# Optimization experiments

Hardware: AMD Instinct MI355X
Metric: run time of the kernel (lower is better)

Reference implementation:

```python
import jax, jax.numpy as jnp
import numpy as np

N = 50000
IN_CH = 256
HEADS = 8
OUT_CH = 32
E = 800000


def setup_inputs() -> dict:
    key = jax.random.key(0)
    k1, k2, k3, k4, k5 = jax.random.split(key, 5)
    x = jax.random.normal(k1, (N, IN_CH), dtype=jnp.float32)
    edge_index = jax.random.randint(k2, (2, E), 0, N, dtype=jnp.int64)
    # torch Linear(in, heads*out, bias=False): weight [heads*out, in]
    W = jax.random.normal(k3, (HEADS * OUT_CH, IN_CH), dtype=jnp.float32) / np.sqrt(IN_CH)
    # xavier_uniform over (1, heads, out)
    bound = float(np.sqrt(6.0 / (HEADS + OUT_CH)))
    attn_l = jax.random.uniform(k4, (1, HEADS, OUT_CH), minval=-bound, maxval=bound, dtype=jnp.float32)
    attn_r = jax.random.uniform(k5, (1, HEADS, OUT_CH), minval=-bound, maxval=bound, dtype=jnp.float32)
    return {"x": x, "edge_index": edge_index, "W": W, "attn_l": attn_l, "attn_r": attn_r}


def reference(x, edge_index, W, attn_l, attn_r):
    num_nodes = x.shape[0]
    # node-level projection: [N, H, C]
    xp = (x @ W.T).reshape(num_nodes, HEADS, OUT_CH).astype(jnp.float32)
    # add self loops
    loops = jnp.arange(num_nodes, dtype=edge_index.dtype)
    src = jnp.concatenate([edge_index[0], loops])
    dst = jnp.concatenate([edge_index[1], loops])
    # edge attention logits per head: [Etot, H]
    alpha_l = (xp * attn_l).sum(-1)[src]
    alpha_r = (xp * attn_r).sum(-1)[dst]
    alpha = jax.nn.leaky_relu(alpha_l + alpha_r, negative_slope=0.2)
    # global per-head max subtraction (as in the original), then scatter softmax over dst
    alpha = jnp.exp(alpha - alpha.max(axis=0, keepdims=True))
    alpha_sum = jax.ops.segment_sum(alpha, dst, num_segments=num_nodes)  # [N, H]
    alpha = alpha / jnp.maximum(alpha_sum[dst], 1e-6)
    # weighted aggregation: scatter-add alpha * x_src to dst, all heads at once
    msgs = alpha[:, :, None] * xp[src]  # [Etot, H, C]
    out = jax.ops.segment_sum(msgs, dst, num_segments=num_nodes)  # [N, H, C]
    return out.reshape(num_nodes, HEADS * OUT_CH)
```

## Files before the change

kernel.cpp:

```cpp
#include <hip/hip_runtime.h>
#include <math.h>

#define IN_CH   256
#define HEADS   8
#define OUT_CH  32
#define CAP     64

typedef __attribute__((ext_vector_type(8))) short s16x8;
typedef __attribute__((ext_vector_type(4))) float f32x4;

__device__ inline short f2bf(float f) {
  unsigned u = __builtin_bit_cast(unsigned, f);
  u += 0x7fffu + ((u >> 16) & 1u);
  return (short)(u >> 16);
}

__global__ __launch_bounds__(256) void prep(
    const float* __restrict__ W, short* __restrict__ Wb,
    int* __restrict__ cnt) {
  const int b = blockIdx.x;
  if (b < 64) {
    const int i = (b * 256 + (int)threadIdx.x) * 4;
    float4 v = *(const float4*)(W + i);
    ushort4 o;
    o.x = (unsigned short)f2bf(v.x);
    o.y = (unsigned short)f2bf(v.y);
    o.z = (unsigned short)f2bf(v.z);
    o.w = (unsigned short)f2bf(v.w);
    *(ushort4*)(Wb + i) = o;
  } else {
    const int i = ((b - 64) * 256 + (int)threadIdx.x) * 4;
    *(int4*)(cnt + i) = make_int4(0, 0, 0, 0);
  }
}

__global__ __launch_bounds__(256) void gemm_fill(
    const float* __restrict__ x, const short* __restrict__ Wb,
    const float* __restrict__ attn_l, const float* __restrict__ attn_r,
    short* __restrict__ xpb, float* __restrict__ al, float* __restrict__ ar,
    const int* __restrict__ src_idx, const int* __restrict__ dst_idx,
    int* __restrict__ cnt, int* __restrict__ csrs, int E, int n) {
  const int tid = threadIdx.x;

  {
    const int Etot = E + n;
    const int stride = (int)gridDim.x * 256;
    for (int e = (int)blockIdx.x * 256 + tid; e < Etot; e += stride) {
      int s, d;
      if (e < E) {
        s = src_idx[e];
        d = dst_idx[e];
      } else {
        s = d = e - E;
      }
      const int p = atomicAdd(&cnt[d], 1);
      if (p < CAP) csrs[d * CAP + p] = s;
    }
  }

  __shared__ short Ws[8 * 256 * 8];
  __shared__ short Xs[8 * 64 * 8];
  const int wave = tid >> 6;
  const int lane = tid & 63;
  const int nrow = lane & 15;
  const int kq   = lane >> 4;
  const int node0 = blockIdx.x * 64;

  f32x4 acc[4][4];
#pragma unroll
  for (int i = 0; i < 4; ++i)
#pragma unroll
    for (int j = 0; j < 4; ++j) acc[i][j] = (f32x4){0.f, 0.f, 0.f, 0.f};

  for (int k0 = 0; k0 < IN_CH; k0 += 64) {
    __syncthreads();
#pragma unroll
    for (int s = 0; s < 8; ++s) {
      s16x8 v = *(const s16x8*)(Wb + (size_t)tid * IN_CH + k0 + s * 8);
      *(s16x8*)&Ws[(s * 256 + tid) * 8] = v;
    }
#pragma unroll
    for (int p = 0; p < 2; ++p) {
      const int c = p * 256 + tid;
      const int row = c >> 3, o = c & 7;
      int grow = node0 + row;
      if (grow >= n) grow = n - 1;
      const float* xr = x + (size_t)grow * IN_CH + k0 + o * 8;
      float4 lo = *(const float4*)xr;
      float4 hi = *(const float4*)(xr + 4);
      s16x8 v;
      v[0] = f2bf(lo.x); v[1] = f2bf(lo.y); v[2] = f2bf(lo.z); v[3] = f2bf(lo.w);
      v[4] = f2bf(hi.x); v[5] = f2bf(hi.y); v[6] = f2bf(hi.z); v[7] = f2bf(hi.w);
      *(s16x8*)&Xs[(o * 64 + row) * 8] = v;
    }
    __syncthreads();
#pragma unroll
    for (int kk = 0; kk < 2; ++kk) {
      const int o = kk * 4 + kq;
      s16x8 af[4], bf[4];
#pragma unroll
      for (int i = 0; i < 4; ++i)
        af[i] = *(const s16x8*)&Ws[(o * 256 + wave * 64 + i * 16 + nrow) * 8];
#pragma unroll
      for (int j = 0; j < 4; ++j)
        bf[j] = *(const s16x8*)&Xs[(o * 64 + j * 16 + nrow) * 8];
#pragma unroll
      for (int i = 0; i < 4; ++i)
#pragma unroll
        for (int j = 0; j < 4; ++j)
          acc[i][j] = __builtin_amdgcn_mfma_f32_16x16x32_bf16(
              af[i], bf[j], acc[i][j], 0, 0, 0);
    }
  }

  float pl[4][2] = {}, pr[4][2] = {};
#pragma unroll
  for (int i = 0; i < 4; ++i) {
    const int oc = wave * 64 + i * 16 + kq * 4;
    const float4 la = *(const float4*)(attn_l + oc);
    const float4 ra = *(const float4*)(attn_r + oc);
    const int hh = i >> 1;
#pragma unroll
    for (int j = 0; j < 4; ++j) {
      const int node = node0 + j * 16 + nrow;
      ushort4 st;
      st.x = (unsigned short)f2bf(acc[i][j][0]);
      st.y = (unsigned short)f2bf(acc[i][j][1]);
      st.z = (unsigned short)f2bf(acc[i][j][2]);
      st.w = (unsigned short)f2bf(acc[i][j][3]);
      if (node < n) *(ushort4*)(xpb + (size_t)node * IN_CH + oc) = st;
      pl[j][hh] += acc[i][j][0] * la.x + acc[i][j][1] * la.y +
                   acc[i][j][2] * la.z + acc[i][j][3] * la.w;
      pr[j][hh] += acc[i][j][0] * ra.x + acc[i][j][1] * ra.y +
                   acc[i][j][2] * ra.z + acc[i][j][3] * ra.w;
    }
  }
#pragma unroll
  for (int j = 0; j < 4; ++j)
#pragma unroll
    for (int hh = 0; hh < 2; ++hh) {
      float vl = pl[j][hh], vr = pr[j][hh];
      vl += __shfl_xor(vl, 16); vl += __shfl_xor(vl, 32);
      vr += __shfl_xor(vr, 16); vr += __shfl_xor(vr, 32);
      const int node = node0 + j * 16 + nrow;
      if (kq == 0 && node < n) {
        al[node * HEADS + wave * 2 + hh] = vl;
        ar[node * HEADS + wave * 2 + hh] = vr;
      }
    }
}

__device__ inline void acc8(float w, const s16x8& u, float* acc) {
  const unsigned* p = (const unsigned*)&u;
#pragma unroll
  for (int j = 0; j < 4; ++j) {
    const unsigned v = p[j];
    const float flo = __builtin_bit_cast(float, v << 16);
    const float fhi = __builtin_bit_cast(float, v & 0xFFFF0000u);
    acc[2 * j]     = fmaf(w, flo, acc[2 * j]);
    acc[2 * j + 1] = fmaf(w, fhi, acc[2 * j + 1]);
  }
}

__global__ __launch_bounds__(256) void gat_gather(
    const int* __restrict__ csrs, const int* __restrict__ cntp,
    const short* __restrict__ xpb, const float* __restrict__ al,
    const float* __restrict__ ar, float* __restrict__ out, int n) {
  const int gid = blockIdx.x * blockDim.x + threadIdx.x;
  const int d = gid >> 6;
  if (d >= n) return;
  const int lane = gid & 63;
  const int half = lane >> 5;
  const int cl = lane & 31;
  const int h = cl >> 2;
  const int start = d * CAP;
  int cnt = cntp[d];
  if (cnt > CAP) cnt = CAP;
  const float ard = ar[d * HEADS + h];

  float acc[8] = {0.f, 0.f, 0.f, 0.f, 0.f, 0.f, 0.f, 0.f};
  float denom = 0.f;
  for (int jb = 0; jb < cnt; jb += 8) {
    const int base = jb + half * 4;
    const int4 q = *(const int4*)(csrs + start + base);
    const int* qp = (const int*)&q;
    int s[4];
#pragma unroll
    for (int i = 0; i < 4; ++i) s[i] = (base + i < cnt) ? qp[i] : d;
    s16x8 u[4];
#pragma unroll
    for (int i = 0; i < 4; ++i)
      u[i] = *(const s16x8*)(xpb + (size_t)s[i] * IN_CH + cl * 8);
    float w[4];
#pragma unroll
    for (int i = 0; i < 4; ++i) {
      float a = al[s[i] * HEADS + h] + ard;
      a = a > 0.f ? a : 0.2f * a;
      w[i] = (base + i < cnt) ? __expf(a) : 0.f;
      denom += w[i];
    }
#pragma unroll
    for (int i = 0; i < 4; ++i) acc8(w[i], u[i], acc);
  }
  denom += __shfl_xor(denom, 32);
#pragma unroll
  for (int k = 0; k < 8; ++k) acc[k] += __shfl_xor(acc[k], 32);
  if (half == 0) {
    const float inv = 1.f / fmaxf(denom, 1e-6f);
    f32x4 v0 = {acc[0] * inv, acc[1] * inv, acc[2] * inv, acc[3] * inv};
    f32x4 v1 = {acc[4] * inv, acc[5] * inv, acc[6] * inv, acc[7] * inv};
    float* op = out + (size_t)d * IN_CH + cl * 8;
    __builtin_nontemporal_store(v0, (f32x4*)op);
    __builtin_nontemporal_store(v1, (f32x4*)(op + 4));
  }
}

extern "C" void kernel_launch(void* const* d_in, const int* in_sizes, int n_in,
                              void* d_out, int out_size, void* d_ws,
                              size_t ws_size, hipStream_t stream) {
  const float* x      = (const float*)d_in[0];
  const int*   ei     = (const int*)d_in[1];
  const float* W      = (const float*)d_in[2];
  const float* attn_l = (const float*)d_in[3];
  const float* attn_r = (const float*)d_in[4];
  float* out = (float*)d_out;

  const int n = in_sizes[0] / IN_CH;
  const int E = in_sizes[1] / 2;

  short* xpb  = (short*)d_ws;
  short* Wb   = xpb + (size_t)n * IN_CH;
  float* al   = (float*)(Wb + IN_CH * IN_CH);
  float* ar   = al + (size_t)n * HEADS;
  int*   cnt  = (int*)(ar + (size_t)n * HEADS);
  int*   csrs = cnt + n;

  prep<<<113, 256, 0, stream>>>(W, Wb, cnt);

  const int gemm_blocks = (n + 63) / 64;
  gemm_fill<<<gemm_blocks, 256, 0, stream>>>(
      x, Wb, attn_l, attn_r, xpb, al, ar, ei, ei + E, cnt, csrs, E, n);

  const long long g_threads = (long long)n * 64;
  gat_gather<<<(int)((g_threads + 255) / 256), 256, 0, stream>>>(
      csrs, cnt, xpb, al, ar, out, n);
}
```

Baseline: 249.5 us.

## Overlap edge fill with GEMM, pre-seed self loops, use direct LDS loads

Self-loop entries are now written in the prep kernel (cnt initialised to 1, csrs slot 0 set to d), so the fill loop only walks the real edges. The fill uses vectorised int4 index loads with four atomics per iteration. Even blocks do the fill before the GEMM and odd blocks after it, which mixes atomic-heavy and MFMA-heavy work across the GPU. W is pre-swizzled into tile order so it can be loaded into LDS with global_load_lds, bypassing registers. The costs are more complex layout code and slot 0 always holding the self loop, which changes which edges are dropped when a node exceeds CAP.

Result: faster. 226.7 us (-9.2%).

```diff
diff --git a/kernel.cpp b/kernel.cpp
--- a/kernel.cpp
+++ b/kernel.cpp
@@ -8,6 +8,8 @@
 
 typedef __attribute__((ext_vector_type(8))) short s16x8;
 typedef __attribute__((ext_vector_type(4))) float f32x4;
+typedef __attribute__((address_space(1))) const unsigned int gu32;
+typedef __attribute__((address_space(3))) unsigned int lu32;
 
 __device__ inline short f2bf(float f) {
   unsigned u = __builtin_bit_cast(unsigned, f);
@@ -16,47 +18,70 @@
 }
 
 __global__ __launch_bounds__(256) void prep(
-    const float* __restrict__ W, short* __restrict__ Wb,
-    int* __restrict__ cnt) {
+    const float* __restrict__ W, short* __restrict__ Wq,
+    int* __restrict__ cnt, int* __restrict__ csrs, int n, int cnt_blocks) {
   const int b = blockIdx.x;
-  if (b < 64) {
-    const int i = (b * 256 + (int)threadIdx.x) * 4;
-    float4 v = *(const float4*)(W + i);
-    ushort4 o;
-    o.x = (unsigned short)f2bf(v.x);
-    o.y = (unsigned short)f2bf(v.y);
-    o.z = (unsigned short)f2bf(v.z);
-    o.w = (unsigned short)f2bf(v.w);
-    *(ushort4*)(Wb + i) = o;
+  const int tid = threadIdx.x;
+  if (b < 32) {
+    const int g = b * 256 + tid;
+    const int oc = g & 255, s = (g >> 8) & 7, t = g >> 11;
+    const float* sp = W + oc * IN_CH + t * 64 + s * 8;
+    float4 lo = *(const float4*)sp;
+    float4 hi = *(const float4*)(sp + 4);
+    s16x8 v;
+    v[0] = f2bf(lo.x); v[1] = f2bf(lo.y); v[2] = f2bf(lo.z); v[3] = f2bf(lo.w);
+    v[4] = f2bf(hi.x); v[5] = f2bf(hi.y); v[6] = f2bf(hi.z); v[7] = f2bf(hi.w);
+    *(s16x8*)&Wq[g * 8] = v;
+  } else if (b < 32 + cnt_blocks) {
+    const int i = ((b - 32) * 256 + tid) * 4;
+    *(int4*)(cnt + i) = make_int4(1, 1, 1, 1);
   } else {
-    const int i = ((b - 64) * 256 + (int)threadIdx.x) * 4;
-    *(int4*)(cnt + i) = make_int4(0, 0, 0, 0);
+    const int d = (b - 32 - cnt_blocks) * 256 + tid;
+    if (d < n) csrs[(size_t)d * CAP] = d;
+  }
+}
+
+__device__ inline void fill_edges(const int* __restrict__ src_idx,
+                                  const int* __restrict__ dst_idx,
+                                  int* __restrict__ cnt,
+                                  int* __restrict__ csrs, int E,
+                                  int tg, int tot) {
+  for (int e = tg * 4; e < E; e += tot * 4) {
+    int ss[4], dd[4];
+    if ((E & 3) == 0 && e + 3 < E) {
+      const int4 a = *(const int4*)(src_idx + e);
+      const int4 b = *(const int4*)(dst_idx + e);
+      ss[0] = a.x; ss[1] = a.y; ss[2] = a.z; ss[3] = a.w;
+      dd[0] = b.x; dd[1] = b.y; dd[2] = b.z; dd[3] = b.w;
+    } else {
+#pragma unroll
+      for (int i = 0; i < 4; ++i) {
+        if (e + i < E) { ss[i] = src_idx[e + i]; dd[i] = dst_idx[e + i]; }
+        else dd[i] = -1;
+      }
+    }
+#pragma unroll
+    for (int i = 0; i < 4; ++i) {
+      if (dd[i] >= 0) {
+        const int p = atomicAdd(&cnt[dd[i]], 1);
+        if (p < CAP) csrs[dd[i] * CAP + p] = ss[i];
+      }
+    }
   }
 }
 
 __global__ __launch_bounds__(256) void gemm_fill(
-    const float* __restrict__ x, const short* __restrict__ Wb,
+    const float* __restrict__ x, const short* __restrict__ Wq,
     const float* __restrict__ attn_l, const float* __restrict__ attn_r,
     short* __restrict__ xpb, float* __restrict__ al, float* __restrict__ ar,
     const int* __restrict__ src_idx, const int* __restrict__ dst_idx,
     int* __restrict__ cnt, int* __restrict__ csrs, int E, int n) {
   const int tid = threadIdx.x;
-
-  {
-    const int Etot = E + n;
-    const int stride = (int)gridDim.x * 256;
-    for (int e = (int)blockIdx.x * 256 + tid; e < Etot; e += stride) {
-      int s, d;
-      if (e < E) {
-        s = src_idx[e];
-        d = dst_idx[e];
-      } else {
-        s = d = e - E;
-      }
-      const int p = atomicAdd(&cnt[d], 1);
-      if (p < CAP) csrs[d * CAP + p] = s;
-    }
-  }
+  const int tg  = (int)blockIdx.x * 256 + tid;
+  const int tot = (int)gridDim.x * 256;
+  const bool fill_first = (blockIdx.x & 1) == 0;
+
+  if (fill_first) fill_edges(src_idx, dst_idx, cnt, csrs, E, tg, tot);
 
   __shared__ short Ws[8 * 256 * 8];
   __shared__ short Xs[8 * 64 * 8];
@@ -72,13 +97,15 @@
 #pragma unroll
     for (int j = 0; j < 4; ++j) acc[i][j] = (f32x4){0.f, 0.f, 0.f, 0.f};
 
-  for (int k0 = 0; k0 < IN_CH; k0 += 64) {
+  for (int t = 0; t < 4; ++t) {
     __syncthreads();
 #pragma unroll
     for (int s = 0; s < 8; ++s) {
-      s16x8 v = *(const s16x8*)(Wb + (size_t)tid * IN_CH + k0 + s * 8);
-      *(s16x8*)&Ws[(s * 256 + tid) * 8] = v;
-    }
+      const short* gp = Wq + ((t * 8 + s) * 256 + tid) * 8;
+      __builtin_amdgcn_global_load_lds(
+          (gu32*)gp, (lu32*)&Ws[(s * 256 + wave * 64) * 8], 16, 0, 0);
+    }
+    const int k0 = t * 64;
 #pragma unroll
     for (int p = 0; p < 2; ++p) {
       const int c = p * 256 + tid;
@@ -148,6 +175,8 @@
         ar[node * HEADS + wave * 2 + hh] = vr;
       }
     }
+
+  if (!fill_first) fill_edges(src_idx, dst_idx, cnt, csrs, E, tg, tot);
 }
 
 __device__ inline void acc8(float w, const s16x8& u, float* acc) {
@@ -229,17 +258,20 @@
   const int E = in_sizes[1] / 2;
 
   short* xpb  = (short*)d_ws;
-  short* Wb   = xpb + (size_t)n * IN_CH;
-  float* al   = (float*)(Wb + IN_CH * IN_CH);
+  short* Wq   = xpb + (size_t)n * IN_CH;
+  float* al   = (float*)(Wq + IN_CH * IN_CH);
   float* ar   = al + (size_t)n * HEADS;
   int*   cnt  = (int*)(ar + (size_t)n * HEADS);
-  int*   csrs = cnt + n;
-
-  prep<<<113, 256, 0, stream>>>(W, Wb, cnt);
+  const int cnt_blocks = (n + 1023) / 1024;
+  int*   csrs = cnt + (size_t)cnt_blocks * 1024;
+
+  const int seed_blocks = (n + 255) / 256;
+  prep<<<32 + cnt_blocks + seed_blocks, 256, 0, stream>>>(
+      W, Wq, cnt, csrs, n, cnt_blocks);
 
   const int gemm_blocks = (n + 63) / 64;
   gemm_fill<<<gemm_blocks, 256, 0, stream>>>(
-      x, Wb, attn_l, attn_r, xpb, al, ar, ei, ei + E, cnt, csrs, E, n);
+      x, Wq, attn_l, attn_r, xpb, al, ar, ei, ei + E, cnt, csrs, E, n);
 
   const long long g_threads = (long long)n * 64;
   gat_gather<<<(int)((g_threads + 255) / 256), 256, 0, stream>>>(
```
